# Kernel optimization log

Hardware: AMD Instinct MI355X
Metric: run time of the kernel (lower is better)

Reference implementation:

```python
import jax, jax.numpy as jnp
import numpy as np

EPS = 1e-6

def _rmsnorm(x, w):
    var = jnp.mean(x * x, axis=-1, keepdims=True)
    return x * jax.lax.rsqrt(var + EPS) * w

def _act_quant(x):
    # per-token int8 absmax quantization (BitNet b1.58)
    scale = 127.0 / jnp.clip(jnp.max(jnp.abs(x), axis=-1, keepdims=True), 1e-5)
    return jnp.round(jnp.clip(x * scale, -128.0, 127.0)) / scale

def _weight_quant(w):
    # per-tensor ternary quantization with mean-abs scale
    scale = 1.0 / jnp.clip(jnp.mean(jnp.abs(w)), 1e-5)
    return jnp.round(jnp.clip(w * scale, -1.0, 1.0)) / scale

def _ste(x, qfn):
    return x + jax.lax.stop_gradient(qfn(x) - x)

def _bitlinear(x, w):
    xq = _ste(x, _act_quant)
    wq = _ste(w, _weight_quant)
    return jnp.einsum('bsh,fh->bsf', xq, wq)

def setup_inputs() -> dict:
    key = jax.random.key(0)
    k1, k2, k3 = jax.random.split(key, 3)
    B, S, H, F = 4, 4096, 1024, 4096
    x = jax.random.normal(k1, (B, S, H), dtype=jnp.float32)
    norm_w = jnp.ones((H,), dtype=jnp.float32)
    w_up = jax.random.normal(k2, (F, H), dtype=jnp.float32) * (H ** -0.5)
    w_down = jax.random.normal(k3, (H, F), dtype=jnp.float32) * (F ** -0.5)
    return {"x": x, "norm_w": norm_w, "w_up": w_up, "w_down": w_down}

def reference(x, norm_w, w_up, w_down):
    residual = x
    h = _rmsnorm(x, norm_w)
    h = _bitlinear(h, w_up)          # [B,S,F]
    h = jnp.square(jax.nn.relu(h))   # relu^2
    h = _bitlinear(h, w_down)        # [B,S,H]
    return h + residual
```

## Files before the change

kernel.cpp:

```cpp
#include <hip/hip_runtime.h>
#include <hip/hip_fp16.h>

#define M_TOK 16384
#define H_DIM 1024
#define F_DIM 4096

typedef __attribute__((ext_vector_type(4))) int int4v;

static const size_t OFF_H2    = 0;
static const size_t OFF_Q2    = OFF_H2   + 134217728ULL;
static const size_t OFF_XQ    = OFF_Q2   + 67108864ULL;
static const size_t OFF_WQU   = OFF_XQ   + 16777216ULL;
static const size_t OFF_WQD   = OFF_WQU  + 4194304ULL;
static const size_t OFF_DQX   = OFF_WQD  + 4194304ULL;
static const size_t OFF_DQ2   = OFF_DQX  + 65536ULL;
static const size_t OFF_PMAX  = OFF_DQ2  + 65536ULL;
static const size_t OFF_WPART = OFF_PMAX + 4194304ULL;
static const size_t OFF_WSC   = OFF_WPART+ 8192ULL;
static const size_t WS_NEEDED = OFF_WSC  + 16ULL;

__device__ __forceinline__ void ldg_lds16(const void* g, void* l) {
  __builtin_amdgcn_global_load_lds(
      (const __attribute__((address_space(1))) void*)g,
      (__attribute__((address_space(3))) void*)l, 16, 0, 0);
}

__global__ __launch_bounds__(256) void k_wabs(const float* __restrict__ wu,
                                              const float* __restrict__ wd,
                                              float* __restrict__ part) {
  const int b = blockIdx.x;
  const float* w = (b < 1024) ? wu : wd;
  const int cb = b & 1023;
  const size_t base = (size_t)cb * 4096 + threadIdx.x * 4;
  float s = 0.0f;
#pragma unroll
  for (int it = 0; it < 4; ++it) {
    const float4 v = *(const float4*)(w + base + it * 1024);
    s += fabsf(v.x) + fabsf(v.y) + fabsf(v.z) + fabsf(v.w);
  }
#pragma unroll
  for (int sh = 32; sh; sh >>= 1) s += __shfl_xor(s, sh, 64);
  __shared__ float red[4];
  if ((threadIdx.x & 63) == 0) red[threadIdx.x >> 6] = s;
  __syncthreads();
  if (threadIdx.x == 0) part[b] = red[0] + red[1] + red[2] + red[3];
}

__global__ __launch_bounds__(256) void k_wscale(const float* __restrict__ part,
                                                float* __restrict__ wsc) {
  const int b = blockIdx.x;
  const float* p = part + b * 1024;
  float s = p[threadIdx.x] + p[threadIdx.x + 256] + p[threadIdx.x + 512] + p[threadIdx.x + 768];
#pragma unroll
  for (int sh = 32; sh; sh >>= 1) s += __shfl_xor(s, sh, 64);
  __shared__ float red[4];
  if ((threadIdx.x & 63) == 0) red[threadIdx.x >> 6] = s;
  __syncthreads();
  if (threadIdx.x == 0) {
    const float mean = (red[0] + red[1] + red[2] + red[3]) * (1.0f / 4194304.0f);
    const float c = fmaxf(mean, 1e-5f);
    wsc[b * 2]     = c;
    wsc[b * 2 + 1] = 1.0f / c;
  }
}

__global__ __launch_bounds__(256) void k_wquant(const float* __restrict__ wu,
                                                const float* __restrict__ wd,
                                                char* __restrict__ qu,
                                                char* __restrict__ qd,
                                                const float* __restrict__ wsc) {
  const size_t t = (size_t)blockIdx.x * 256 + threadIdx.x;
  const float* w; char* q; float scale; size_t i;
  if (t < 1048576) { w = wu; q = qu; scale = wsc[1]; i = t * 4; }
  else             { w = wd; q = qd; scale = wsc[3]; i = (t - 1048576) * 4; }
  const float4 v = *(const float4*)(w + i);
  const int a = (int)rintf(fminf(fmaxf(v.x * scale, -1.0f), 1.0f));
  const int b = (int)rintf(fminf(fmaxf(v.y * scale, -1.0f), 1.0f));
  const int c = (int)rintf(fminf(fmaxf(v.z * scale, -1.0f), 1.0f));
  const int d = (int)rintf(fminf(fmaxf(v.w * scale, -1.0f), 1.0f));
  *(unsigned*)(q + i) = (a & 255) | ((b & 255) << 8) | ((c & 255) << 16) | ((d & 255) << 24);
}

__global__ __launch_bounds__(256) void k_rmsnorm_quant(const float* __restrict__ x,
                                                       const float* __restrict__ nw,
                                                       char* __restrict__ xq,
                                                       float* __restrict__ dqx) {
  const int row = blockIdx.x;
  const int t = threadIdx.x;
  const float4 v = *(const float4*)(x + (size_t)row * H_DIM + t * 4);
  float ss = v.x * v.x + v.y * v.y + v.z * v.z + v.w * v.w;
#pragma unroll
  for (int sh = 32; sh; sh >>= 1) ss += __shfl_xor(ss, sh, 64);
  __shared__ float red[4];
  __shared__ float redm[4];
  if ((t & 63) == 0) red[t >> 6] = ss;
  __syncthreads();
  ss = red[0] + red[1] + red[2] + red[3];
  const float rinv = 1.0f / sqrtf(ss * (1.0f / 1024.0f) + 1e-6f);
  const float4 w4 = *(const float4*)(nw + t * 4);
  float4 n;
  n.x = v.x * rinv * w4.x;  n.y = v.y * rinv * w4.y;
  n.z = v.z * rinv * w4.z;  n.w = v.w * rinv * w4.w;
  float am = fmaxf(fmaxf(fabsf(n.x), fabsf(n.y)), fmaxf(fabsf(n.z), fabsf(n.w)));
#pragma unroll
  for (int sh = 32; sh; sh >>= 1) am = fmaxf(am, __shfl_xor(am, sh, 64));
  if ((t & 63) == 0) redm[t >> 6] = am;
  __syncthreads();
  am = fmaxf(fmaxf(redm[0], redm[1]), fmaxf(redm[2], redm[3]));
  am = fmaxf(am, 1e-5f);
  const float scale = 127.0f / am;
  const int qa = (int)rintf(fminf(fmaxf(n.x * scale, -128.0f), 127.0f));
  const int qb = (int)rintf(fminf(fmaxf(n.y * scale, -128.0f), 127.0f));
  const int qc = (int)rintf(fminf(fmaxf(n.z * scale, -128.0f), 127.0f));
  const int qd = (int)rintf(fminf(fmaxf(n.w * scale, -128.0f), 127.0f));
  *(unsigned*)(xq + (size_t)row * H_DIM + t * 4) =
      (qa & 255) | ((qb & 255) << 8) | ((qc & 255) << 16) | ((qd & 255) << 24);
  if (t == 0) dqx[row] = am * (1.0f / 127.0f);
}

template <int LD>
__device__ __forceinline__ void stage4(const char* g, char* l) {
  ldg_lds16(g,                     l);
  ldg_lds16(g + (size_t)64  * LD,  l + 8192);
  ldg_lds16(g + (size_t)128 * LD,  l + 16384);
  ldg_lds16(g + (size_t)192 * LD,  l + 24576);
}

template <int LDA_, int LDB_, int KT>
__device__ __forceinline__ void gemm_core256(const char* __restrict__ A,
                                             const char* __restrict__ B,
                                             int mBase, int nBase,
                                             char* __restrict__ smem,
                                             int4v acc[8][4]) {
  const int t = threadIdx.x;
  const int lane = t & 63;
  const int w = t >> 6;
  const int wm = w & 1;
  const int wn = w >> 1;
  const int sRow = t >> 3;
  const int sSeg = (t & 7) ^ (sRow & 7);
  const char* Ag = A + (size_t)(mBase + sRow) * LDA_ + sSeg * 16;
  const char* Bg = B + (size_t)(nBase + sRow) * LDB_ + sSeg * 16;
  const int q  = lane >> 4;
  const int fr = lane & 15;
  const int sw = fr & 7;

  stage4<LDA_>(Ag, smem + (t << 4));
  stage4<LDB_>(Bg, smem + 32768 + (t << 4));
  __syncthreads();

  int cur = 0;
  for (int kt = 0; kt < KT; ++kt) {
    const int nxt = cur ^ 65536;
    const char* Ab = smem + cur + wm * 16384;
    const char* Bb = smem + cur + 32768 + wn * 8192;
    int4v a[8], b[4];
    if (kt + 1 < KT) stage4<LDA_>(Ag + (size_t)(kt + 1) * 128, smem + nxt + (t << 4));
    {
      const int ao = ((q ^ sw) << 4);
#pragma unroll
      for (int i = 0; i < 8; ++i) a[i] = *(const int4v*)(Ab + (i * 16 + fr) * 128 + ao);
#pragma unroll
      for (int j = 0; j < 4; ++j) b[j] = *(const int4v*)(Bb + (j * 16 + fr) * 128 + ao);
    }
    __builtin_amdgcn_s_barrier();
    __builtin_amdgcn_s_setprio(1);
#pragma unroll
    for (int i = 0; i < 8; ++i)
#pragma unroll
      for (int j = 0; j < 4; ++j)
        acc[i][j] = __builtin_amdgcn_mfma_i32_16x16x64_i8(a[i], b[j], acc[i][j], 0, 0, 0);
    __builtin_amdgcn_s_setprio(0);
    if (kt + 1 < KT) stage4<LDB_>(Bg + (size_t)(kt + 1) * 128, smem + nxt + 32768 + (t << 4));
    {
      const int ao = (((4 + q) ^ sw) << 4);
#pragma unroll
      for (int i = 0; i < 8; ++i) a[i] = *(const int4v*)(Ab + (i * 16 + fr) * 128 + ao);
#pragma unroll
      for (int j = 0; j < 4; ++j) b[j] = *(const int4v*)(Bb + (j * 16 + fr) * 128 + ao);
    }
    __builtin_amdgcn_s_barrier();
    __builtin_amdgcn_s_setprio(1);
#pragma unroll
    for (int i = 0; i < 8; ++i)
#pragma unroll
      for (int j = 0; j < 4; ++j)
        acc[i][j] = __builtin_amdgcn_mfma_i32_16x16x64_i8(a[i], b[j], acc[i][j], 0, 0, 0);
    __builtin_amdgcn_s_setprio(0);
    __syncthreads();
    cur = nxt;
  }
}

__global__ __launch_bounds__(512, 2) void k_gemm1(const char* __restrict__ xq,
                                                  const char* __restrict__ wq,
                                                  const float* __restrict__ wsc,
                                                  const float* __restrict__ dqx,
                                                  __half* __restrict__ h2,
                                                  float* __restrict__ pmax) {
  __shared__ char smem[131072];
  int4v acc[8][4];
#pragma unroll
  for (int i = 0; i < 8; ++i)
#pragma unroll
    for (int j = 0; j < 4; ++j) acc[i][j] = (int4v){0, 0, 0, 0};
  const int mBase = blockIdx.x * 256;
  const int nBase = blockIdx.y * 256;
  gemm_core256<H_DIM, H_DIM, 8>(xq, wq, mBase, nBase, smem, acc);

  const int t = threadIdx.x;
  const int lane = t & 63;
  const int w = t >> 6;
  const int wm = w & 1;
  const int wn = w >> 1;
  const int q  = lane >> 4;
  const int fr = lane & 15;
  const float dqw = wsc[0];
#pragma unroll
  for (int i = 0; i < 8; ++i) {
    const int rbase = mBase + wm * 128 + i * 16 + (q << 2);
    const float4 dq4 = *(const float4*)(dqx + rbase);
    const float* dqp = (const float*)&dq4;
    float rmax[4] = {0.0f, 0.0f, 0.0f, 0.0f};
#pragma unroll
    for (int j = 0; j < 4; ++j) {
      const int col = nBase + wn * 64 + j * 16 + fr;
#pragma unroll
      for (int r = 0; r < 4; ++r) {
        float v = (float)acc[i][j][r] * dqp[r] * dqw;
        v = fmaxf(v, 0.0f);
        v = v * v;
        const __half h = __float2half(v);
        h2[(size_t)(rbase + r) * F_DIM + col] = h;
        rmax[r] = fmaxf(rmax[r], __half2float(h));
      }
    }
#pragma unroll
    for (int s = 1; s < 16; s <<= 1) {
#pragma unroll
      for (int r = 0; r < 4; ++r) rmax[r] = fmaxf(rmax[r], __shfl_xor(rmax[r], s, 64));
    }
    if (fr == 0) {
      const int nb2 = blockIdx.y * 4 + wn;
#pragma unroll
      for (int r = 0; r < 4; ++r) pmax[(size_t)nb2 * M_TOK + rbase + r] = rmax[r];
    }
  }
}

__global__ __launch_bounds__(256) void k_quant2(const __half* __restrict__ h2,
                                                const float* __restrict__ pmax,
                                                char* __restrict__ q2,
                                                float* __restrict__ dq2) {
  const int row = blockIdx.x;
  const int t = threadIdx.x;
  __shared__ float sm;
  if (t < 64) {
    float m = pmax[(size_t)t * M_TOK + row];
#pragma unroll
    for (int sh = 32; sh; sh >>= 1) m = fmaxf(m, __shfl_xor(m, sh, 64));
    if (t == 0) sm = fmaxf(m, 1e-5f);
  }
  __syncthreads();
  const float mx = sm;
  const float s = 127.0f / mx;
  if (t == 0) dq2[row] = mx * (1.0f / 127.0f);
  const size_t i = (size_t)row * F_DIM + t * 16;
  __half2 hh[8];
  *(float4*)(hh)     = *(const float4*)(h2 + i);
  *(float4*)(hh + 4) = *(const float4*)(h2 + i + 8);
  unsigned u[4];
#pragma unroll
  for (int k = 0; k < 4; ++k) {
    const int q0 = (int)rintf(fminf(__low2float(hh[2 * k]) * s, 127.0f));
    const int q1 = (int)rintf(fminf(__high2float(hh[2 * k]) * s, 127.0f));
    const int q2i = (int)rintf(fminf(__low2float(hh[2 * k + 1]) * s, 127.0f));
    const int q3 = (int)rintf(fminf(__high2float(hh[2 * k + 1]) * s, 127.0f));
    u[k] = (q0 & 255) | ((q1 & 255) << 8) | ((q2i & 255) << 16) | ((q3 & 255) << 24);
  }
  *(uint4*)(q2 + i) = make_uint4(u[0], u[1], u[2], u[3]);
}

__global__ __launch_bounds__(512, 2) void k_gemm2(const char* __restrict__ q2,
                                                  const char* __restrict__ wq,
                                                  const float* __restrict__ wsc,
                                                  const float* __restrict__ dq2,
                                                  const float* __restrict__ x,
                                                  float* __restrict__ out) {
  __shared__ char smem[131072];
  int4v acc[8][4];
#pragma unroll
  for (int i = 0; i < 8; ++i)
#pragma unroll
    for (int j = 0; j < 4; ++j) acc[i][j] = (int4v){0, 0, 0, 0};
  const int mBase = blockIdx.x * 256;
  const int nBase = blockIdx.y * 256;
  gemm_core256<F_DIM, F_DIM, 32>(q2, wq, mBase, nBase, smem, acc);

  const int t = threadIdx.x;
  const int lane = t & 63;
  const int w = t >> 6;
  const int wm = w & 1;
  const int wn = w >> 1;
  const int q  = lane >> 4;
  const int fr = lane & 15;
  const float dqw = wsc[2];
#pragma unroll
  for (int i = 0; i < 8; ++i) {
    const int rbase = mBase + wm * 128 + i * 16 + (q << 2);
    const float4 dq4 = *(const float4*)(dq2 + rbase);
    const float* dqp = (const float*)&dq4;
#pragma unroll
    for (int j = 0; j < 4; ++j) {
      const int col = nBase + wn * 64 + j * 16 + fr;
#pragma unroll
      for (int r = 0; r < 4; ++r) {
        const size_t idx = (size_t)(rbase + r) * H_DIM + col;
        out[idx] = (float)acc[i][j][r] * dqp[r] * dqw + x[idx];
      }
    }
  }
}

extern "C" void kernel_launch(void* const* d_in, const int* in_sizes, int n_in,
                              void* d_out, int out_size, void* d_ws, size_t ws_size,
                              hipStream_t stream) {
  const float* x  = (const float*)d_in[0];
  const float* nw = (const float*)d_in[1];
  const float* wu = (const float*)d_in[2];
  const float* wd = (const float*)d_in[3];
  float* out = (float*)d_out;
  char* ws = (char*)d_ws;
  if (ws_size < WS_NEEDED) return;

  __half* h2     = (__half*)(ws + OFF_H2);
  char* q2       = ws + OFF_Q2;
  char* xq       = ws + OFF_XQ;
  char* wqu      = ws + OFF_WQU;
  char* wqd      = ws + OFF_WQD;
  float* dqx     = (float*)(ws + OFF_DQX);
  float* dq2     = (float*)(ws + OFF_DQ2);
  float* pmax    = (float*)(ws + OFF_PMAX);
  float* wpart   = (float*)(ws + OFF_WPART);
  float* wsc     = (float*)(ws + OFF_WSC);

  k_wabs<<<2048, 256, 0, stream>>>(wu, wd, wpart);
  k_wscale<<<2, 256, 0, stream>>>(wpart, wsc);
  k_wquant<<<8192, 256, 0, stream>>>(wu, wd, wqu, wqd, wsc);
  k_rmsnorm_quant<<<M_TOK, 256, 0, stream>>>(x, nw, xq, dqx);
  k_gemm1<<<dim3(M_TOK / 256, F_DIM / 256), 512, 0, stream>>>(xq, wqu, wsc, dqx, h2, pmax);
  k_quant2<<<M_TOK, 256, 0, stream>>>(h2, pmax, q2, dq2);
  k_gemm2<<<dim3(M_TOK / 256, H_DIM / 256), 512, 0, stream>>>(q2, wqd, wsc, dq2, x, out);
}
```

Before: 340.3 us.

## Rework int8 GEMM mainloop into 4-stage 64-wide K pipeline with split loads

Measured after the change: 363.7 us. +6.9%, slower.

```diff
diff --git a/kernel.cpp b/kernel.cpp
--- a/kernel.cpp
+++ b/kernel.cpp
@@ -119,76 +119,86 @@
 }
 
 template <int LD>
-__device__ __forceinline__ void stage4(const char* g, char* l) {
-  ldg_lds16(g,                     l);
-  ldg_lds16(g + (size_t)64  * LD,  l + 8192);
-  ldg_lds16(g + (size_t)128 * LD,  l + 16384);
-  ldg_lds16(g + (size_t)192 * LD,  l + 24576);
-}
+__device__ __forceinline__ void stage_half(const char* g, char* l) {
+  ldg_lds16(g, l);
+  ldg_lds16(g + (size_t)128 * LD, l + 8192);
+}
+
+#define MFMA_I8(i, j, av, bv) \
+  acc[i][j] = __builtin_amdgcn_mfma_i32_16x16x64_i8(av, bv, acc[i][j], 0, 0, 0)
 
 template <int LDA_, int LDB_, int KT>
-__device__ __forceinline__ void gemm_core256(const char* __restrict__ A,
-                                             const char* __restrict__ B,
-                                             int mBase, int nBase,
-                                             char* __restrict__ smem,
-                                             int4v acc[8][4]) {
+__device__ __forceinline__ void gemm_core64(const char* __restrict__ A,
+                                            const char* __restrict__ B,
+                                            int mBase, int nBase,
+                                            char* __restrict__ smem,
+                                            int4v acc[8][4]) {
   const int t = threadIdx.x;
   const int lane = t & 63;
   const int w = t >> 6;
   const int wm = w & 1;
   const int wn = w >> 1;
-  const int sRow = t >> 3;
-  const int sSeg = (t & 7) ^ (sRow & 7);
-  const char* Ag = A + (size_t)(mBase + sRow) * LDA_ + sSeg * 16;
-  const char* Bg = B + (size_t)(nBase + sRow) * LDB_ + sSeg * 16;
+  const int sr = t >> 2;
+  const int sG = (t & 3) ^ (sr & 3);
+  const char* Ag = A + (size_t)(mBase + sr) * LDA_ + sG * 16;
+  const char* Bg = B + (size_t)(nBase + sr) * LDB_ + sG * 16;
   const int q  = lane >> 4;
   const int fr = lane & 15;
-  const int sw = fr & 7;
-
-  stage4<LDA_>(Ag, smem + (t << 4));
-  stage4<LDB_>(Bg, smem + 32768 + (t << 4));
-  __syncthreads();
-
-  int cur = 0;
+  const int aoff = ((q ^ (fr & 3)) << 4);
+  const int rA = wm * 128 + fr;
+  const int rB = wn * 64 + fr;
+  char* ldst = smem + (t << 4);
+
+  stage_half<LDA_>(Ag,       ldst);
+  stage_half<LDA_>(Ag + 64,  ldst + 32768);
+  stage_half<LDB_>(Bg,       ldst + 16384);
+  stage_half<LDA_>(Ag + 128, ldst + 65536);
+  stage_half<LDB_>(Bg + 64,  ldst + 32768 + 16384);
+  asm volatile("s_waitcnt vmcnt(4)" ::: "memory");
+  __builtin_amdgcn_s_barrier();
+
   for (int kt = 0; kt < KT; ++kt) {
-    const int nxt = cur ^ 65536;
-    const char* Ab = smem + cur + wm * 16384;
-    const char* Bb = smem + cur + 32768 + wn * 8192;
-    int4v a[8], b[4];
-    if (kt + 1 < KT) stage4<LDA_>(Ag + (size_t)(kt + 1) * 128, smem + nxt + (t << 4));
-    {
-      const int ao = ((q ^ sw) << 4);
-#pragma unroll
-      for (int i = 0; i < 8; ++i) a[i] = *(const int4v*)(Ab + (i * 16 + fr) * 128 + ao);
-#pragma unroll
-      for (int j = 0; j < 4; ++j) b[j] = *(const int4v*)(Bb + (j * 16 + fr) * 128 + ao);
-    }
+    const char* bb = smem + (kt & 3) * 32768;
+    int4v a0 = *(const int4v*)(bb + (rA +   0) * 64 + aoff);
+    int4v a1 = *(const int4v*)(bb + (rA +  16) * 64 + aoff);
+    int4v a2 = *(const int4v*)(bb + (rA +  32) * 64 + aoff);
+    int4v a3 = *(const int4v*)(bb + (rA +  48) * 64 + aoff);
+    int4v b0 = *(const int4v*)(bb + 16384 + (rB +  0) * 64 + aoff);
+    int4v b1 = *(const int4v*)(bb + 16384 + (rB + 16) * 64 + aoff);
+    int4v b2 = *(const int4v*)(bb + 16384 + (rB + 32) * 64 + aoff);
+    int4v b3 = *(const int4v*)(bb + 16384 + (rB + 48) * 64 + aoff);
+    if (kt + 3 < KT)
+      stage_half<LDA_>(Ag + (size_t)(kt + 3) * 64,
+                       smem + ((kt + 3) & 3) * 32768 + (t << 4));
     __builtin_amdgcn_s_barrier();
+    asm volatile("s_waitcnt lgkmcnt(0)" ::: "memory");
+    __builtin_amdgcn_sched_barrier(0);
     __builtin_amdgcn_s_setprio(1);
-#pragma unroll
-    for (int i = 0; i < 8; ++i)
-#pragma unroll
-      for (int j = 0; j < 4; ++j)
-        acc[i][j] = __builtin_amdgcn_mfma_i32_16x16x64_i8(a[i], b[j], acc[i][j], 0, 0, 0);
+    MFMA_I8(0, 0, a0, b0); MFMA_I8(0, 1, a0, b1); MFMA_I8(0, 2, a0, b2); MFMA_I8(0, 3, a0, b3);
+    MFMA_I8(1, 0, a1, b0); MFMA_I8(1, 1, a1, b1); MFMA_I8(1, 2, a1, b2); MFMA_I8(1, 3, a1, b3);
+    MFMA_I8(2, 0, a2, b0); MFMA_I8(2, 1, a2, b1); MFMA_I8(2, 2, a2, b2); MFMA_I8(2, 3, a2, b3);
+    MFMA_I8(3, 0, a3, b0); MFMA_I8(3, 1, a3, b1); MFMA_I8(3, 2, a3, b2); MFMA_I8(3, 3, a3, b3);
     __builtin_amdgcn_s_setprio(0);
-    if (kt + 1 < KT) stage4<LDB_>(Bg + (size_t)(kt + 1) * 128, smem + nxt + 32768 + (t << 4));
-    {
-      const int ao = (((4 + q) ^ sw) << 4);
-#pragma unroll
-      for (int i = 0; i < 8; ++i) a[i] = *(const int4v*)(Ab + (i * 16 + fr) * 128 + ao);
-#pragma unroll
-      for (int j = 0; j < 4; ++j) b[j] = *(const int4v*)(Bb + (j * 16 + fr) * 128 + ao);
-    }
+    a0 = *(const int4v*)(bb + (rA +  64) * 64 + aoff);
+    a1 = *(const int4v*)(bb + (rA +  80) * 64 + aoff);
+    a2 = *(const int4v*)(bb + (rA +  96) * 64 + aoff);
+    a3 = *(const int4v*)(bb + (rA + 112) * 64 + aoff);
+    if (kt + 2 < KT)
+      stage_half<LDB_>(Bg + (size_t)(kt + 2) * 64,
+                       smem + ((kt + 2) & 3) * 32768 + 16384 + (t << 4));
     __builtin_amdgcn_s_barrier();
+    asm volatile("s_waitcnt lgkmcnt(0)" ::: "memory");
+    __builtin_amdgcn_sched_barrier(0);
     __builtin_amdgcn_s_setprio(1);
-#pragma unroll
-    for (int i = 0; i < 8; ++i)
-#pragma unroll
-      for (int j = 0; j < 4; ++j)
-        acc[i][j] = __builtin_amdgcn_mfma_i32_16x16x64_i8(a[i], b[j], acc[i][j], 0, 0, 0);
+    MFMA_I8(4, 0, a0, b0); MFMA_I8(4, 1, a0, b1); MFMA_I8(4, 2, a0, b2); MFMA_I8(4, 3, a0, b3);
+    MFMA_I8(5, 0, a1, b0); MFMA_I8(5, 1, a1, b1); MFMA_I8(5, 2, a1, b2); MFMA_I8(5, 3, a1, b3);
+    MFMA_I8(6, 0, a2, b0); MFMA_I8(6, 1, a2, b1); MFMA_I8(6, 2, a2, b2); MFMA_I8(6, 3, a2, b3);
+    MFMA_I8(7, 0, a3, b0); MFMA_I8(7, 1, a3, b1); MFMA_I8(7, 2, a3, b2); MFMA_I8(7, 3, a3, b3);
     __builtin_amdgcn_s_setprio(0);
-    __syncthreads();
-    cur = nxt;
+    if (kt + 3 < KT)      { asm volatile("s_waitcnt vmcnt(4)" ::: "memory"); }
+    else if (kt + 2 < KT) { asm volatile("s_waitcnt vmcnt(2)" ::: "memory"); }
+    else                  { asm volatile("s_waitcnt vmcnt(0)" ::: "memory"); }
+    __builtin_amdgcn_s_barrier();
   }
 }
 
@@ -206,7 +216,7 @@
     for (int j = 0; j < 4; ++j) acc[i][j] = (int4v){0, 0, 0, 0};
   const int mBase = blockIdx.x * 256;
   const int nBase = blockIdx.y * 256;
-  gemm_core256<H_DIM, H_DIM, 8>(xq, wq, mBase, nBase, smem, acc);
+  gemm_core64<H_DIM, H_DIM, 16>(xq, wq, mBase, nBase, smem, acc);
 
   const int t = threadIdx.x;
   const int lane = t & 63;
@@ -295,7 +305,7 @@
     for (int j = 0; j < 4; ++j) acc[i][j] = (int4v){0, 0, 0, 0};
   const int mBase = blockIdx.x * 256;
   const int nBase = blockIdx.y * 256;
-  gemm_core256<F_DIM, F_DIM, 32>(q2, wq, mBase, nBase, smem, acc);
+  gemm_core64<F_DIM, F_DIM, 64>(q2, wq, mBase, nBase, smem, acc);
 
   const int t = threadIdx.x;
   const int lane = t & 63;
```

## Split GEMM k-step into four phases with interleaved async loads and vmcnt waits

Applied to the files above, without the earlier changes.

New measurement: 333.8 us. No clear change (-1.9%).

```diff
diff --git a/kernel.cpp b/kernel.cpp
--- a/kernel.cpp
+++ b/kernel.cpp
@@ -118,20 +118,23 @@
   if (t == 0) dqx[row] = am * (1.0f / 127.0f);
 }
 
-template <int LD>
-__device__ __forceinline__ void stage4(const char* g, char* l) {
-  ldg_lds16(g,                     l);
-  ldg_lds16(g + (size_t)64  * LD,  l + 8192);
-  ldg_lds16(g + (size_t)128 * LD,  l + 16384);
-  ldg_lds16(g + (size_t)192 * LD,  l + 24576);
-}
+#define MFMA_I8(i, j, av, bv) \
+  acc[i][j] = __builtin_amdgcn_mfma_i32_16x16x64_i8(av, bv, acc[i][j], 0, 0, 0)
+
+#define MFMA16(IB) \
+  __builtin_amdgcn_s_setprio(1); \
+  MFMA_I8(IB + 0, 0, a0, b0); MFMA_I8(IB + 0, 1, a0, b1); MFMA_I8(IB + 0, 2, a0, b2); MFMA_I8(IB + 0, 3, a0, b3); \
+  MFMA_I8(IB + 1, 0, a1, b0); MFMA_I8(IB + 1, 1, a1, b1); MFMA_I8(IB + 1, 2, a1, b2); MFMA_I8(IB + 1, 3, a1, b3); \
+  MFMA_I8(IB + 2, 0, a2, b0); MFMA_I8(IB + 2, 1, a2, b1); MFMA_I8(IB + 2, 2, a2, b2); MFMA_I8(IB + 2, 3, a2, b3); \
+  MFMA_I8(IB + 3, 0, a3, b0); MFMA_I8(IB + 3, 1, a3, b1); MFMA_I8(IB + 3, 2, a3, b2); MFMA_I8(IB + 3, 3, a3, b3); \
+  __builtin_amdgcn_s_setprio(0)
 
 template <int LDA_, int LDB_, int KT>
-__device__ __forceinline__ void gemm_core256(const char* __restrict__ A,
-                                             const char* __restrict__ B,
-                                             int mBase, int nBase,
-                                             char* __restrict__ smem,
-                                             int4v acc[8][4]) {
+__device__ __forceinline__ void gemm_core4p(const char* __restrict__ A,
+                                            const char* __restrict__ B,
+                                            int mBase, int nBase,
+                                            char* __restrict__ smem,
+                                            int4v acc[8][4]) {
   const int t = threadIdx.x;
   const int lane = t & 63;
   const int w = t >> 6;
@@ -144,52 +147,68 @@
   const int q  = lane >> 4;
   const int fr = lane & 15;
   const int sw = fr & 7;
-
-  stage4<LDA_>(Ag, smem + (t << 4));
-  stage4<LDB_>(Bg, smem + 32768 + (t << 4));
-  __syncthreads();
+  const int s0 = ((q) ^ sw) << 4;
+  const int s1 = ((4 + q) ^ sw) << 4;
+  const int rA = wm * 128 + fr;
+  const int rB = wn * 64 + fr;
+  const int dst = t << 4;
+
+#define STG_A(Q, KTI, BUFO) \
+  ldg_lds16(Ag + (size_t)((Q) * 64) * LDA_ + (size_t)(KTI) * 128, \
+            smem + (BUFO) + (Q) * 8192 + dst)
+#define STG_B(Q, KTI, BUFO) \
+  ldg_lds16(Bg + (size_t)((Q) * 64) * LDB_ + (size_t)(KTI) * 128, \
+            smem + (BUFO) + 32768 + (Q) * 8192 + dst)
+
+  STG_B(0, 0, 0); STG_B(1, 0, 0); STG_B(2, 0, 0); STG_B(3, 0, 0);
+  STG_A(0, 0, 0); STG_A(2, 0, 0); STG_A(1, 0, 0); STG_A(3, 0, 0);
+  asm volatile("s_waitcnt vmcnt(2)\n\ts_barrier" ::: "memory");
 
   int cur = 0;
   for (int kt = 0; kt < KT; ++kt) {
     const int nxt = cur ^ 65536;
-    const char* Ab = smem + cur + wm * 16384;
-    const char* Bb = smem + cur + 32768 + wn * 8192;
-    int4v a[8], b[4];
-    if (kt + 1 < KT) stage4<LDA_>(Ag + (size_t)(kt + 1) * 128, smem + nxt + (t << 4));
-    {
-      const int ao = ((q ^ sw) << 4);
-#pragma unroll
-      for (int i = 0; i < 8; ++i) a[i] = *(const int4v*)(Ab + (i * 16 + fr) * 128 + ao);
-#pragma unroll
-      for (int j = 0; j < 4; ++j) b[j] = *(const int4v*)(Bb + (j * 16 + fr) * 128 + ao);
-    }
-    __builtin_amdgcn_s_barrier();
-    __builtin_amdgcn_s_setprio(1);
-#pragma unroll
-    for (int i = 0; i < 8; ++i)
-#pragma unroll
-      for (int j = 0; j < 4; ++j)
-        acc[i][j] = __builtin_amdgcn_mfma_i32_16x16x64_i8(a[i], b[j], acc[i][j], 0, 0, 0);
-    __builtin_amdgcn_s_setprio(0);
-    if (kt + 1 < KT) stage4<LDB_>(Bg + (size_t)(kt + 1) * 128, smem + nxt + 32768 + (t << 4));
-    {
-      const int ao = (((4 + q) ^ sw) << 4);
-#pragma unroll
-      for (int i = 0; i < 8; ++i) a[i] = *(const int4v*)(Ab + (i * 16 + fr) * 128 + ao);
-#pragma unroll
-      for (int j = 0; j < 4; ++j) b[j] = *(const int4v*)(Bb + (j * 16 + fr) * 128 + ao);
-    }
-    __builtin_amdgcn_s_barrier();
-    __builtin_amdgcn_s_setprio(1);
-#pragma unroll
-    for (int i = 0; i < 8; ++i)
-#pragma unroll
-      for (int j = 0; j < 4; ++j)
-        acc[i][j] = __builtin_amdgcn_mfma_i32_16x16x64_i8(a[i], b[j], acc[i][j], 0, 0, 0);
-    __builtin_amdgcn_s_setprio(0);
-    __syncthreads();
+    const char* Ab = smem + cur;
+    const char* Bb = smem + cur + 32768;
+    int4v a0, a1, a2, a3, b0, b1, b2, b3;
+    a0 = *(const int4v*)(Ab + (rA +  0) * 128 + s0);
+    a1 = *(const int4v*)(Ab + (rA + 16) * 128 + s0);
+    a2 = *(const int4v*)(Ab + (rA + 32) * 128 + s0);
+    a3 = *(const int4v*)(Ab + (rA + 48) * 128 + s0);
+    b0 = *(const int4v*)(Bb + (rB +  0) * 128 + s0);
+    b1 = *(const int4v*)(Bb + (rB + 16) * 128 + s0);
+    b2 = *(const int4v*)(Bb + (rB + 32) * 128 + s0);
+    b3 = *(const int4v*)(Bb + (rB + 48) * 128 + s0);
+    if (kt + 1 < KT) { STG_B(0, kt + 1, nxt); STG_B(1, kt + 1, nxt); }
+    MFMA16(0);
+    if (kt + 1 < KT) { asm volatile("s_waitcnt vmcnt(2)\n\ts_barrier" ::: "memory"); }
+    else             { asm volatile("s_waitcnt vmcnt(0)\n\ts_barrier" ::: "memory"); }
+    a0 = *(const int4v*)(Ab + (rA +  64) * 128 + s0);
+    a1 = *(const int4v*)(Ab + (rA +  80) * 128 + s0);
+    a2 = *(const int4v*)(Ab + (rA +  96) * 128 + s0);
+    a3 = *(const int4v*)(Ab + (rA + 112) * 128 + s0);
+    if (kt + 1 < KT) { STG_B(2, kt + 1, nxt); STG_B(3, kt + 1, nxt); }
+    MFMA16(4);
+    a0 = *(const int4v*)(Ab + (rA +  0) * 128 + s1);
+    a1 = *(const int4v*)(Ab + (rA + 16) * 128 + s1);
+    a2 = *(const int4v*)(Ab + (rA + 32) * 128 + s1);
+    a3 = *(const int4v*)(Ab + (rA + 48) * 128 + s1);
+    b0 = *(const int4v*)(Bb + (rB +  0) * 128 + s1);
+    b1 = *(const int4v*)(Bb + (rB + 16) * 128 + s1);
+    b2 = *(const int4v*)(Bb + (rB + 32) * 128 + s1);
+    b3 = *(const int4v*)(Bb + (rB + 48) * 128 + s1);
+    if (kt + 1 < KT) { STG_A(0, kt + 1, nxt); STG_A(2, kt + 1, nxt); }
+    MFMA16(0);
+    a0 = *(const int4v*)(Ab + (rA +  64) * 128 + s1);
+    a1 = *(const int4v*)(Ab + (rA +  80) * 128 + s1);
+    a2 = *(const int4v*)(Ab + (rA +  96) * 128 + s1);
+    a3 = *(const int4v*)(Ab + (rA + 112) * 128 + s1);
+    if (kt + 1 < KT) { STG_A(1, kt + 1, nxt); STG_A(3, kt + 1, nxt); }
+    MFMA16(4);
+    asm volatile("s_waitcnt vmcnt(2)\n\ts_barrier" ::: "memory");
     cur = nxt;
   }
+#undef STG_A
+#undef STG_B
 }
 
 __global__ __launch_bounds__(512, 2) void k_gemm1(const char* __restrict__ xq,
@@ -206,7 +225,7 @@
     for (int j = 0; j < 4; ++j) acc[i][j] = (int4v){0, 0, 0, 0};
   const int mBase = blockIdx.x * 256;
   const int nBase = blockIdx.y * 256;
-  gemm_core256<H_DIM, H_DIM, 8>(xq, wq, mBase, nBase, smem, acc);
+  gemm_core4p<H_DIM, H_DIM, 8>(xq, wq, mBase, nBase, smem, acc);
 
   const int t = threadIdx.x;
   const int lane = t & 63;
@@ -295,7 +314,7 @@
     for (int j = 0; j < 4; ++j) acc[i][j] = (int4v){0, 0, 0, 0};
   const int mBase = blockIdx.x * 256;
   const int nBase = blockIdx.y * 256;
-  gemm_core256<F_DIM, F_DIM, 32>(q2, wq, mBase, nBase, smem, acc);
+  gemm_core4p<F_DIM, F_DIM, 32>(q2, wq, mBase, nBase, smem, acc);
 
   const int t = threadIdx.x;
   const int lane = t & 63;
```
